# Optimization experiments

Measured on AMD Instinct MI355X. Metric: run time of the kernel, lower is better.

Reference implementation:

```python
import jax, jax.numpy as jnp
import numpy as np

N_NODES = 50000

def gcn_conv(x, W, b, row, col, ew, n):
    # PyG GCNConv: linear first (no bias in lin), then gcn_norm with added
    # self-loops (weight 1.0), symmetric D^{-1/2} normalization, scatter-add
    # aggregation from row (source) to col (target), then bias.
    h = x @ W                                      # [N, out]
    loop = jnp.arange(n, dtype=row.dtype)
    row_f = jnp.concatenate([row, loop])
    col_f = jnp.concatenate([col, loop])
    ew_f = jnp.concatenate([ew, jnp.ones((n,), dtype=ew.dtype)])
    deg = jax.ops.segment_sum(ew_f, col_f, num_segments=n)
    dinv = jnp.where(deg > 0, jax.lax.rsqrt(jnp.maximum(deg, 1e-30)), 0.0)
    norm = dinv[row_f] * ew_f * dinv[col_f]        # [E+N]
    msg = norm[:, None] * h[row_f]                 # gather + scale
    out = jax.ops.segment_sum(msg, col_f, num_segments=n)  # scatter-add
    return out + b

def setup_inputs() -> dict:
    key = jax.random.key(0)
    k = jax.random.split(key, 8)
    in_dim, hidden_dim, out_dim = 128, 256, 128
    n, e = N_NODES, 600000
    x = jax.random.normal(k[0], (n, in_dim), dtype=jnp.float32)
    edge_index = jax.random.randint(k[1], (2, e), 0, n, dtype=jnp.int64)
    edge_weight = jax.random.uniform(k[2], (e,), dtype=jnp.float32)
    # Glorot-style params (PyG GCNConv lin has no bias; bias added after aggregation)
    W1 = jax.random.normal(k[3], (in_dim, hidden_dim), dtype=jnp.float32) / np.sqrt(in_dim)
    b1 = jnp.zeros((hidden_dim,), dtype=jnp.float32)
    W2 = jax.random.normal(k[4], (hidden_dim, out_dim), dtype=jnp.float32) / np.sqrt(hidden_dim)
    b2 = jnp.zeros((out_dim,), dtype=jnp.float32)
    return {"x": x, "edge_index": edge_index, "edge_weight": edge_weight,
            "W1": W1, "b1": b1, "W2": W2, "b2": b2}

def reference(x, edge_index, edge_weight, W1, b1, W2, b2):
    n = x.shape[0]
    row, col = edge_index[0], edge_index[1]
    h = jax.nn.relu(gcn_conv(x, W1, b1, row, col, edge_weight, n))
    # dropout is identity in eval mode
    out = jax.nn.relu(gcn_conv(h, W2, b2, row, col, edge_weight, n))
    return out
```

## Files before the change

kernel.cpp:

```cpp
#include <hip/hip_runtime.h>
#include <hip/hip_bf16.h>

constexpr int IN_DIM  = 128;
constexpr int HID     = 256;
constexpr int OUT_DIM = 128;
constexpr int ELL_W   = 64;

typedef __attribute__((ext_vector_type(8))) short short8;
typedef __attribute__((ext_vector_type(8))) unsigned short ushort8;
typedef __attribute__((ext_vector_type(4))) float f32x4;

__device__ __forceinline__ float bf2f(unsigned short u) {
    return __uint_as_float(((unsigned int)u) << 16);
}
__device__ __forceinline__ unsigned short f2bf(float f) {
    unsigned int u = __float_as_uint(f);
    u += 0x7FFFu + ((u >> 16) & 1u);
    return (unsigned short)(u >> 16);
}

__global__ void k_zero(int* __restrict__ cnt, int n) {
    int i = blockIdx.x * blockDim.x + threadIdx.x;
    if (i < n) cnt[i] = 0;
}

__global__ void k_fill_ell(const int* __restrict__ row, const int* __restrict__ col,
                           const float* __restrict__ ew, int* __restrict__ cnt,
                           int2* __restrict__ ell, int E) {
    int e = blockIdx.x * blockDim.x + threadIdx.x;
    if (e < E) {
        const int c = col[e];
        const int pos = atomicAdd(&cnt[c], 1);
        if (pos < ELL_W)
            ell[(size_t)c * ELL_W + pos] = make_int2(row[e], __float_as_int(ew[e]));
    }
}

__global__ __launch_bounds__(256)
void k_deg(const int* __restrict__ cnt, const int2* __restrict__ ell,
           float* __restrict__ dinv, int n) {
    constexpr int LPN = 8;
    const int node = blockIdx.x * (256 / LPN) + threadIdx.x / LPN;
    const int l = threadIdx.x % LPN;
    if (node >= n) return;
    const int m = min(cnt[node], ELL_W);
    const int2* b = ell + (size_t)node * ELL_W;
    float s = 0.f;
    for (int p = l; p < m; p += LPN) s += __int_as_float(b[p].y);
    #pragma unroll
    for (int d = 4; d; d >>= 1) s += __shfl_xor(s, d, LPN);
    if (l == 0) dinv[node] = rsqrtf(1.0f + s);
}

__global__ void k_coef(const int* __restrict__ cnt, int2* __restrict__ ell,
                       const float* __restrict__ dinv, int n) {
    int idx = blockIdx.x * blockDim.x + threadIdx.x;
    if (idx >= n * ELL_W) return;
    const int node = idx >> 6;
    const int slot = idx & (ELL_W - 1);
    if (slot < min(cnt[node], ELL_W)) {
        int2 m = ell[idx];
        ell[idx].y = __float_as_int(dinv[m.x] * __int_as_float(m.y));
    }
}

__global__ void k_x2bf(const float* __restrict__ x, unsigned short* __restrict__ xb,
                       size_t total4) {
    size_t i = (size_t)blockIdx.x * blockDim.x + threadIdx.x;
    if (i < total4) {
        const float4 v = *reinterpret_cast<const float4*>(x + i * 4);
        ushort o[4] = {f2bf(v.x), f2bf(v.y), f2bf(v.z), f2bf(v.w)};
        *reinterpret_cast<uint2*>(xb + i * 4) = *reinterpret_cast<uint2*>(o);
    }
}

__global__ void k_wt(const float* __restrict__ W, unsigned short* __restrict__ Wt,
                     int K, int N) {
    int idx = blockIdx.x * blockDim.x + threadIdx.x;
    if (idx < K * N) {
        int k = idx / N, nn = idx % N;
        Wt[(size_t)nn * K + k] = f2bf(W[idx]);
    }
}

template<bool BIAS_RELU, bool BF16OUT>
__global__ __launch_bounds__(256)
void k_gather_bf(const int* __restrict__ cnt, const int2* __restrict__ ell,
                 const float* __restrict__ dinv, const unsigned short* __restrict__ h,
                 const float* __restrict__ bias, void* __restrict__ out_, int n) {
    constexpr int F = 128, TPN = 16, NPB = 256 / TPN;
    const int node = blockIdx.x * NPB + threadIdx.x / TPN;
    const int j8   = (threadIdx.x % TPN) * 8;
    if (node >= n) return;

    const float dc = dinv[node];
    float acc[8];
    {
        const ushort8 hv = *reinterpret_cast<const ushort8*>(h + (size_t)node * F + j8);
        #pragma unroll
        for (int i = 0; i < 8; ++i) acc[i] = dc * bf2f(hv[i]);
    }

    const int2* bucket = ell + (size_t)node * ELL_W;
    const int m = min(cnt[node], ELL_W);
    int p = 0;
    for (; p + 1 < m; p += 2) {
        const int2 m0 = bucket[p], m1 = bucket[p + 1];
        const ushort8 v0 = *reinterpret_cast<const ushort8*>(h + (size_t)m0.x * F + j8);
        const ushort8 v1 = *reinterpret_cast<const ushort8*>(h + (size_t)m1.x * F + j8);
        const float w0 = __int_as_float(m0.y), w1 = __int_as_float(m1.y);
        #pragma unroll
        for (int i = 0; i < 8; ++i) acc[i] = fmaf(w0, bf2f(v0[i]), acc[i]);
        #pragma unroll
        for (int i = 0; i < 8; ++i) acc[i] = fmaf(w1, bf2f(v1[i]), acc[i]);
    }
    if (p < m) {
        const int2 m0 = bucket[p];
        const ushort8 v0 = *reinterpret_cast<const ushort8*>(h + (size_t)m0.x * F + j8);
        const float w0 = __int_as_float(m0.y);
        #pragma unroll
        for (int i = 0; i < 8; ++i) acc[i] = fmaf(w0, bf2f(v0[i]), acc[i]);
    }

    float o[8];
    if (BIAS_RELU) {
        const float4 b0 = *reinterpret_cast<const float4*>(bias + j8);
        const float4 b1 = *reinterpret_cast<const float4*>(bias + j8 + 4);
        const float bb[8] = {b0.x, b0.y, b0.z, b0.w, b1.x, b1.y, b1.z, b1.w};
        #pragma unroll
        for (int i = 0; i < 8; ++i) o[i] = fmaxf(fmaf(dc, acc[i], bb[i]), 0.f);
    } else {
        #pragma unroll
        for (int i = 0; i < 8; ++i) o[i] = dc * acc[i];
    }

    if (BF16OUT) {
        ushort ob[8];
        #pragma unroll
        for (int i = 0; i < 8; ++i) ob[i] = f2bf(o[i]);
        *reinterpret_cast<uint4*>((unsigned short*)out_ + (size_t)node * F + j8) =
            *reinterpret_cast<uint4*>(ob);
    } else {
        float* op = (float*)out_ + (size_t)node * F + j8;
        *reinterpret_cast<float4*>(op)     = make_float4(o[0], o[1], o[2], o[3]);
        *reinterpret_cast<float4*>(op + 4) = make_float4(o[4], o[5], o[6], o[7]);
    }
}

template<bool BIAS_RELU, bool BF16OUT>
__global__ __launch_bounds__(256)
void k_mfma_gemm(const unsigned short* __restrict__ A,
                 const unsigned short* __restrict__ Bt,
                 const float* __restrict__ bias,
                 void* __restrict__ C_, int M, int N, int K) {
    __shared__ ushort As[128 * 64];
    __shared__ ushort Bs[128 * 64];

    const int t    = threadIdx.x;
    const int w    = t >> 6;
    const int lane = t & 63;
    const int quad = lane >> 4;
    const int l16  = lane & 15;
    const int wm   = w >> 1;
    const int wn   = w & 1;
    const int rowBase = blockIdx.y * 128;
    const int colBase = blockIdx.x * 128;

    const ushort* gA = A  + (size_t)(rowBase + w * 32 + lane / 8) * K + (lane % 8) * 8;
    const ushort* gB = Bt + (size_t)(colBase + w * 32 + lane / 8) * K + (lane % 8) * 8;
    ushort* lA = &As[(w * 32) * 64];
    ushort* lB = &Bs[(w * 32) * 64];

    f32x4 acc[4][4] = {};

    for (int k0 = 0; k0 < K; k0 += 64) {
        #pragma unroll
        for (int j = 0; j < 4; ++j) {
            __builtin_amdgcn_global_load_lds(
                (const __attribute__((address_space(1))) uint32_t*)(gA + k0 + (size_t)j * 8 * K),
                (__attribute__((address_space(3))) uint32_t*)(lA + j * 8 * 64), 16, 0, 0);
            __builtin_amdgcn_global_load_lds(
                (const __attribute__((address_space(1))) uint32_t*)(gB + k0 + (size_t)j * 8 * K),
                (__attribute__((address_space(3))) uint32_t*)(lB + j * 8 * 64), 16, 0, 0);
        }
        __syncthreads();

        #pragma unroll
        for (int ks = 0; ks < 2; ++ks) {
            short8 af[4], bf[4];
            #pragma unroll
            for (int mt = 0; mt < 4; ++mt)
                af[mt] = *(const short8*)&As[(wm * 64 + mt * 16 + l16) * 64 + ks * 32 + quad * 8];
            #pragma unroll
            for (int nt = 0; nt < 4; ++nt)
                bf[nt] = *(const short8*)&Bs[(wn * 64 + nt * 16 + l16) * 64 + ks * 32 + quad * 8];
            #pragma unroll
            for (int mt = 0; mt < 4; ++mt)
                #pragma unroll
                for (int nt = 0; nt < 4; ++nt)
                    acc[mt][nt] = __builtin_amdgcn_mfma_f32_16x16x32_bf16(
                        af[mt], bf[nt], acc[mt][nt], 0, 0, 0);
        }
        __syncthreads();
    }

    float bv[4];
    if (BIAS_RELU) {
        #pragma unroll
        for (int nt = 0; nt < 4; ++nt)
            bv[nt] = bias[colBase + wn * 64 + nt * 16 + l16];
    }
    #pragma unroll
    for (int mt = 0; mt < 4; ++mt) {
        #pragma unroll
        for (int i = 0; i < 4; ++i) {
            const int r = rowBase + wm * 64 + mt * 16 + quad * 4 + i;
            if (r < M) {
                #pragma unroll
                for (int nt = 0; nt < 4; ++nt) {
                    const int c = colBase + wn * 64 + nt * 16 + l16;
                    float v = acc[mt][nt][i];
                    if (BIAS_RELU) v = fmaxf(v + bv[nt], 0.f);
                    if (BF16OUT)
                        ((unsigned short*)C_)[(size_t)r * N + c] = f2bf(v);
                    else
                        ((float*)C_)[(size_t)r * N + c] = v;
                }
            }
        }
    }
}

extern "C" void kernel_launch(void* const* d_in, const int* in_sizes, int n_in,
                              void* d_out, int out_size, void* d_ws, size_t ws_size,
                              hipStream_t stream) {
    const float* x  = (const float*)d_in[0];
    const int*   ei = (const int*)d_in[1];
    const float* ew = (const float*)d_in[2];
    const float* W1 = (const float*)d_in[3];
    const float* b1 = (const float*)d_in[4];
    const float* W2 = (const float*)d_in[5];
    const float* b2 = (const float*)d_in[6];
    float* out = (float*)d_out;

    const int n = in_sizes[0] / IN_DIM;
    const int E = in_sizes[1] / 2;
    const int Mpad = (n + 127) & ~127;
    const int* row = ei;
    const int* col = ei + E;

    float* ws = (float*)d_ws;
    size_t o = 0;
    auto alloc = [&](size_t words) { float* p = ws + o; o += (words + 63) & ~(size_t)63; return p; };
    float* dinv = alloc(n);
    int*   cnt  = (int*)alloc(n);
    int2*  ell  = (int2*)alloc((size_t)n * ELL_W * 2);
    unsigned short* xb   = (unsigned short*)alloc((size_t)Mpad * IN_DIM / 2);
    unsigned short* aggx = (unsigned short*)alloc((size_t)Mpad * IN_DIM / 2);
    unsigned short* h1   = (unsigned short*)alloc((size_t)Mpad * HID / 2);
    unsigned short* h2   = (unsigned short*)alloc((size_t)Mpad * OUT_DIM / 2);
    unsigned short* w1t  = (unsigned short*)alloc((size_t)IN_DIM * HID / 2);
    unsigned short* w2t  = (unsigned short*)alloc((size_t)HID * OUT_DIM / 2);

    k_zero<<<(n + 255) / 256, 256, 0, stream>>>(cnt, n);
    k_fill_ell<<<(E + 255) / 256, 256, 0, stream>>>(row, col, ew, cnt, ell, E);
    k_deg<<<(n * 8 + 255) / 256, 256, 0, stream>>>(cnt, ell, dinv, n);
    k_coef<<<(n * ELL_W + 255) / 256, 256, 0, stream>>>(cnt, ell, dinv, n);

    k_x2bf<<<(int)(((size_t)n * IN_DIM / 4 + 255) / 256), 256, 0, stream>>>(x, xb, (size_t)n * IN_DIM / 4);
    k_wt<<<(IN_DIM * HID + 255) / 256, 256, 0, stream>>>(W1, w1t, IN_DIM, HID);
    k_wt<<<(HID * OUT_DIM + 255) / 256, 256, 0, stream>>>(W2, w2t, HID, OUT_DIM);

    k_gather_bf<false, true><<<(n + 15) / 16, 256, 0, stream>>>(cnt, ell, dinv, xb, nullptr, aggx, n);
    {
        dim3 grid(HID / 128, Mpad / 128);
        k_mfma_gemm<true, true><<<grid, 256, 0, stream>>>(aggx, w1t, b1, h1, n, HID, IN_DIM);
    }

    {
        dim3 grid(OUT_DIM / 128, Mpad / 128);
        k_mfma_gemm<false, true><<<grid, 256, 0, stream>>>(h1, w2t, nullptr, h2, n, OUT_DIM, HID);
    }
    k_gather_bf<true, false><<<(n + 15) / 16, 256, 0, stream>>>(cnt, ell, dinv, h2, b2, out, n);
}
```

Before: 219.5 us.

## Prescale features by dinv, fuse prep kernels, split gather edges across wave

Moves the source-side D^{-1/2} factor out of the per-edge coefficient and into the features. x is prescaled during the degree kernel, and h2 is prescaled in the second GEMM epilogue. This drops the separate k_coef pass over the ELL array and the standalone bf16-conversion kernel. Zeroing and weight transposes are merged into one prep kernel, which cuts the launch count. The gather now gives each node a full wave, with four lane groups splitting its edges and reducing them via shuffles, to get more memory-level parallelism per node. The cost is cross-lane reductions and idle lanes in the final write.

```diff
diff --git a/kernel.cpp b/kernel.cpp
--- a/kernel.cpp
+++ b/kernel.cpp
@@ -19,9 +19,19 @@
     return (unsigned short)(u >> 16);
 }
 
-__global__ void k_zero(int* __restrict__ cnt, int n) {
-    int i = blockIdx.x * blockDim.x + threadIdx.x;
+__global__ void k_prep(int* __restrict__ cnt, int n,
+                       const float* __restrict__ W1, unsigned short* __restrict__ w1t,
+                       const float* __restrict__ W2, unsigned short* __restrict__ w2t) {
+    const int i = blockIdx.x * 256 + threadIdx.x;
     if (i < n) cnt[i] = 0;
+    if (i < IN_DIM * HID) {
+        const int k = i / HID, nn = i % HID;
+        w1t[(size_t)nn * IN_DIM + k] = f2bf(W1[i]);
+    }
+    if (i < HID * OUT_DIM) {
+        const int k = i / OUT_DIM, nn = i % OUT_DIM;
+        w2t[(size_t)nn * HID + k] = f2bf(W2[i]);
+    }
 }
 
 __global__ void k_fill_ell(const int* __restrict__ row, const int* __restrict__ col,
@@ -37,77 +47,47 @@
 }
 
 __global__ __launch_bounds__(256)
-void k_deg(const int* __restrict__ cnt, const int2* __restrict__ ell,
-           float* __restrict__ dinv, int n) {
-    constexpr int LPN = 8;
-    const int node = blockIdx.x * (256 / LPN) + threadIdx.x / LPN;
-    const int l = threadIdx.x % LPN;
+void k_deg_xs(const int* __restrict__ cnt, const int2* __restrict__ ell,
+              const float* __restrict__ x, float* __restrict__ dinv,
+              unsigned short* __restrict__ xs, int n) {
+    const int wave = threadIdx.x >> 6;
+    const int lane = threadIdx.x & 63;
+    const int node = blockIdx.x * 4 + wave;
     if (node >= n) return;
     const int m = min(cnt[node], ELL_W);
-    const int2* b = ell + (size_t)node * ELL_W;
-    float s = 0.f;
-    for (int p = l; p < m; p += LPN) s += __int_as_float(b[p].y);
+    float s = (lane < m) ? __int_as_float(ell[(size_t)node * ELL_W + lane].y) : 0.f;
     #pragma unroll
-    for (int d = 4; d; d >>= 1) s += __shfl_xor(s, d, LPN);
-    if (l == 0) dinv[node] = rsqrtf(1.0f + s);
-}
-
-__global__ void k_coef(const int* __restrict__ cnt, int2* __restrict__ ell,
-                       const float* __restrict__ dinv, int n) {
-    int idx = blockIdx.x * blockDim.x + threadIdx.x;
-    if (idx >= n * ELL_W) return;
-    const int node = idx >> 6;
-    const int slot = idx & (ELL_W - 1);
-    if (slot < min(cnt[node], ELL_W)) {
-        int2 m = ell[idx];
-        ell[idx].y = __float_as_int(dinv[m.x] * __int_as_float(m.y));
-    }
-}
-
-__global__ void k_x2bf(const float* __restrict__ x, unsigned short* __restrict__ xb,
-                       size_t total4) {
-    size_t i = (size_t)blockIdx.x * blockDim.x + threadIdx.x;
-    if (i < total4) {
-        const float4 v = *reinterpret_cast<const float4*>(x + i * 4);
-        ushort o[4] = {f2bf(v.x), f2bf(v.y), f2bf(v.z), f2bf(v.w)};
-        *reinterpret_cast<uint2*>(xb + i * 4) = *reinterpret_cast<uint2*>(o);
-    }
-}
-
-__global__ void k_wt(const float* __restrict__ W, unsigned short* __restrict__ Wt,
-                     int K, int N) {
-    int idx = blockIdx.x * blockDim.x + threadIdx.x;
-    if (idx < K * N) {
-        int k = idx / N, nn = idx % N;
-        Wt[(size_t)nn * K + k] = f2bf(W[idx]);
-    }
+    for (int d = 32; d; d >>= 1) s += __shfl_xor(s, d);
+    const float di = rsqrtf(1.0f + s);
+    if (lane == 0) dinv[node] = di;
+    const float2 v = *reinterpret_cast<const float2*>(x + (size_t)node * IN_DIM + lane * 2);
+    const unsigned int packed = (unsigned int)f2bf(v.x * di) |
+                                ((unsigned int)f2bf(v.y * di) << 16);
+    *reinterpret_cast<unsigned int*>(xs + (size_t)node * IN_DIM + lane * 2) = packed;
 }
 
 template<bool BIAS_RELU, bool BF16OUT>
 __global__ __launch_bounds__(256)
-void k_gather_bf(const int* __restrict__ cnt, const int2* __restrict__ ell,
-                 const float* __restrict__ dinv, const unsigned short* __restrict__ h,
-                 const float* __restrict__ bias, void* __restrict__ out_, int n) {
-    constexpr int F = 128, TPN = 16, NPB = 256 / TPN;
-    const int node = blockIdx.x * NPB + threadIdx.x / TPN;
-    const int j8   = (threadIdx.x % TPN) * 8;
+void k_gather_w(const int* __restrict__ cnt, const int2* __restrict__ ell,
+                const float* __restrict__ dinv, const unsigned short* __restrict__ hs,
+                const float* __restrict__ bias, void* __restrict__ out_, int n) {
+    constexpr int F = 128;
+    const int wave  = threadIdx.x >> 6;
+    const int lane  = threadIdx.x & 63;
+    const int group = lane >> 4;
+    const int j8    = (lane & 15) * 8;
+    const int node  = blockIdx.x * 4 + wave;
     if (node >= n) return;
 
-    const float dc = dinv[node];
-    float acc[8];
-    {
-        const ushort8 hv = *reinterpret_cast<const ushort8*>(h + (size_t)node * F + j8);
-        #pragma unroll
-        for (int i = 0; i < 8; ++i) acc[i] = dc * bf2f(hv[i]);
-    }
-
+    const int m = min(cnt[node], ELL_W);
     const int2* bucket = ell + (size_t)node * ELL_W;
-    const int m = min(cnt[node], ELL_W);
-    int p = 0;
-    for (; p + 1 < m; p += 2) {
-        const int2 m0 = bucket[p], m1 = bucket[p + 1];
-        const ushort8 v0 = *reinterpret_cast<const ushort8*>(h + (size_t)m0.x * F + j8);
-        const ushort8 v1 = *reinterpret_cast<const ushort8*>(h + (size_t)m1.x * F + j8);
+
+    float acc[8] = {};
+    int p = group;
+    for (; p + 4 < m; p += 8) {
+        const int2 m0 = bucket[p], m1 = bucket[p + 4];
+        const ushort8 v0 = *reinterpret_cast<const ushort8*>(hs + (size_t)m0.x * F + j8);
+        const ushort8 v1 = *reinterpret_cast<const ushort8*>(hs + (size_t)m1.x * F + j8);
         const float w0 = __int_as_float(m0.y), w1 = __int_as_float(m1.y);
         #pragma unroll
         for (int i = 0; i < 8; ++i) acc[i] = fmaf(w0, bf2f(v0[i]), acc[i]);
@@ -116,43 +96,53 @@
     }
     if (p < m) {
         const int2 m0 = bucket[p];
-        const ushort8 v0 = *reinterpret_cast<const ushort8*>(h + (size_t)m0.x * F + j8);
+        const ushort8 v0 = *reinterpret_cast<const ushort8*>(hs + (size_t)m0.x * F + j8);
         const float w0 = __int_as_float(m0.y);
         #pragma unroll
         for (int i = 0; i < 8; ++i) acc[i] = fmaf(w0, bf2f(v0[i]), acc[i]);
     }
 
-    float o[8];
-    if (BIAS_RELU) {
-        const float4 b0 = *reinterpret_cast<const float4*>(bias + j8);
-        const float4 b1 = *reinterpret_cast<const float4*>(bias + j8 + 4);
-        const float bb[8] = {b0.x, b0.y, b0.z, b0.w, b1.x, b1.y, b1.z, b1.w};
-        #pragma unroll
-        for (int i = 0; i < 8; ++i) o[i] = fmaxf(fmaf(dc, acc[i], bb[i]), 0.f);
-    } else {
-        #pragma unroll
-        for (int i = 0; i < 8; ++i) o[i] = dc * acc[i];
-    }
-
-    if (BF16OUT) {
-        ushort ob[8];
-        #pragma unroll
-        for (int i = 0; i < 8; ++i) ob[i] = f2bf(o[i]);
-        *reinterpret_cast<uint4*>((unsigned short*)out_ + (size_t)node * F + j8) =
-            *reinterpret_cast<uint4*>(ob);
-    } else {
-        float* op = (float*)out_ + (size_t)node * F + j8;
-        *reinterpret_cast<float4*>(op)     = make_float4(o[0], o[1], o[2], o[3]);
-        *reinterpret_cast<float4*>(op + 4) = make_float4(o[4], o[5], o[6], o[7]);
-    }
-}
-
-template<bool BIAS_RELU, bool BF16OUT>
+    #pragma unroll
+    for (int i = 0; i < 8; ++i) {
+        acc[i] += __shfl_xor(acc[i], 16);
+        acc[i] += __shfl_xor(acc[i], 32);
+    }
+
+    if (group == 0) {
+        const float dc = dinv[node];
+        const ushort8 hv = *reinterpret_cast<const ushort8*>(hs + (size_t)node * F + j8);
+        float o[8];
+        if (BIAS_RELU) {
+            const float4 b0 = *reinterpret_cast<const float4*>(bias + j8);
+            const float4 b1 = *reinterpret_cast<const float4*>(bias + j8 + 4);
+            const float bb[8] = {b0.x, b0.y, b0.z, b0.w, b1.x, b1.y, b1.z, b1.w};
+            #pragma unroll
+            for (int i = 0; i < 8; ++i)
+                o[i] = fmaxf(fmaf(dc, acc[i] + bf2f(hv[i]), bb[i]), 0.f);
+        } else {
+            #pragma unroll
+            for (int i = 0; i < 8; ++i) o[i] = dc * (acc[i] + bf2f(hv[i]));
+        }
+        if (BF16OUT) {
+            ushort ob[8];
+            #pragma unroll
+            for (int i = 0; i < 8; ++i) ob[i] = f2bf(o[i]);
+            *reinterpret_cast<uint4*>((unsigned short*)out_ + (size_t)node * F + j8) =
+                *reinterpret_cast<uint4*>(ob);
+        } else {
+            float* op = (float*)out_ + (size_t)node * F + j8;
+            *reinterpret_cast<float4*>(op)     = make_float4(o[0], o[1], o[2], o[3]);
+            *reinterpret_cast<float4*>(op + 4) = make_float4(o[4], o[5], o[6], o[7]);
+        }
+    }
+}
+
+template<bool BIAS_RELU, bool ROWSCALE>
 __global__ __launch_bounds__(256)
 void k_mfma_gemm(const unsigned short* __restrict__ A,
                  const unsigned short* __restrict__ Bt,
-                 const float* __restrict__ bias,
-                 void* __restrict__ C_, int M, int N, int K) {
+                 const float* __restrict__ bias, const float* __restrict__ dinv,
+                 unsigned short* __restrict__ C, int M, int N, int K) {
     __shared__ ushort As[128 * 64];
     __shared__ ushort Bs[128 * 64];
 
@@ -216,15 +206,14 @@
         for (int i = 0; i < 4; ++i) {
             const int r = rowBase + wm * 64 + mt * 16 + quad * 4 + i;
             if (r < M) {
+                const float dr = ROWSCALE ? dinv[r] : 1.0f;
                 #pragma unroll
                 for (int nt = 0; nt < 4; ++nt) {
                     const int c = colBase + wn * 64 + nt * 16 + l16;
                     float v = acc[mt][nt][i];
                     if (BIAS_RELU) v = fmaxf(v + bv[nt], 0.f);
-                    if (BF16OUT)
-                        ((unsigned short*)C_)[(size_t)r * N + c] = f2bf(v);
-                    else
-                        ((float*)C_)[(size_t)r * N + c] = v;
+                    if (ROWSCALE)  v *= dr;
+                    C[(size_t)r * N + c] = f2bf(v);
                 }
             }
         }
@@ -255,31 +244,26 @@
     float* dinv = alloc(n);
     int*   cnt  = (int*)alloc(n);
     int2*  ell  = (int2*)alloc((size_t)n * ELL_W * 2);
-    unsigned short* xb   = (unsigned short*)alloc((size_t)Mpad * IN_DIM / 2);
+    unsigned short* xs   = (unsigned short*)alloc((size_t)Mpad * IN_DIM / 2);
     unsigned short* aggx = (unsigned short*)alloc((size_t)Mpad * IN_DIM / 2);
     unsigned short* h1   = (unsigned short*)alloc((size_t)Mpad * HID / 2);
-    unsigned short* h2   = (unsigned short*)alloc((size_t)Mpad * OUT_DIM / 2);
+    unsigned short* h2s  = (unsigned short*)alloc((size_t)Mpad * OUT_DIM / 2);
     unsigned short* w1t  = (unsigned short*)alloc((size_t)IN_DIM * HID / 2);
     unsigned short* w2t  = (unsigned short*)alloc((size_t)HID * OUT_DIM / 2);
 
-    k_zero<<<(n + 255) / 256, 256, 0, stream>>>(cnt, n);
+    k_prep<<<(n + 255) / 256, 256, 0, stream>>>(cnt, n, W1, w1t, W2, w2t);
     k_fill_ell<<<(E + 255) / 256, 256, 0, stream>>>(row, col, ew, cnt, ell, E);
-    k_deg<<<(n * 8 + 255) / 256, 256, 0, stream>>>(cnt, ell, dinv, n);
-    k_coef<<<(n * ELL_W + 255) / 256, 256, 0, stream>>>(cnt, ell, dinv, n);
-
-    k_x2bf<<<(int)(((size_t)n * IN_DIM / 4 + 255) / 256), 256, 0, stream>>>(x, xb, (size_t)n * IN_DIM / 4);
-    k_wt<<<(IN_DIM * HID + 255) / 256, 256, 0, stream>>>(W1, w1t, IN_DIM, HID);
-    k_wt<<<(HID * OUT_DIM + 255) / 256, 256, 0, stream>>>(W2, w2t, HID, OUT_DIM);
-
-    k_gather_bf<false, true><<<(n + 15) / 16, 256, 0, stream>>>(cnt, ell, dinv, xb, nullptr, aggx, n);
+    k_deg_xs<<<(n + 3) / 4, 256, 0, stream>>>(cnt, ell, x, dinv, xs, n);
+
+    k_gather_w<false, true><<<(n + 3) / 4, 256, 0, stream>>>(cnt, ell, dinv, xs, nullptr, aggx, n);
     {
         dim3 grid(HID / 128, Mpad / 128);
-        k_mfma_gemm<true, true><<<grid, 256, 0, stream>>>(aggx, w1t, b1, h1, n, HID, IN_DIM);
+        k_mfma_gemm<true, false><<<grid, 256, 0, stream>>>(aggx, w1t, b1, nullptr, h1, n, HID, IN_DIM);
     }
 
     {
         dim3 grid(OUT_DIM / 128, Mpad / 128);
-        k_mfma_gemm<false, true><<<grid, 256, 0, stream>>>(h1, w2t, nullptr, h2, n, OUT_DIM, HID);
-    }
-    k_gather_bf<true, false><<<(n + 15) / 16, 256, 0, stream>>>(cnt, ell, dinv, h2, b2, out, n);
-}
+        k_mfma_gemm<false, true><<<grid, 256, 0, stream>>>(h1, w2t, nullptr, dinv, h2s, n, OUT_DIM, HID);
+    }
+    k_gather_w<true, false><<<(n + 3) / 4, 256, 0, stream>>>(cnt, ell, dinv, h2s, b2, out, n);
+}
```

Result: no change. 215.8 us (-1.7%).
